# Performance work log

Measured on AMD Instinct MI355X. Metric: run time of the kernel, lower is better.

The kernel has to match this reference:

```python
import jax, jax.numpy as jnp
import numpy as np
from jax import lax

D_MODEL = 768
D_STATE = 64
BATCH = 2
SEQ = 2048


def setup_inputs() -> dict:
    key = jax.random.key(0)
    ks = jax.random.split(key, 12)
    d, n = D_MODEL, D_STATE
    x = jax.random.normal(ks[0], (BATCH, SEQ, d), dtype=jnp.float32)
    ln_gamma = jnp.ones((d,), jnp.float32)
    ln_beta = jnp.zeros((d,), jnp.float32)
    # nn.Linear default init ~ U(-1/sqrt(d), 1/sqrt(d))
    s = 1.0 / np.sqrt(d)
    W_in = jax.random.uniform(ks[1], (d, d), jnp.float32, -s, s)
    b_in = jax.random.uniform(ks[2], (d,), jnp.float32, -s, s)
    log_A = jax.random.normal(ks[3], (d, n), jnp.float32)
    B_p = jax.random.normal(ks[4], (d, n), jnp.float32) * 0.1
    C_p = jax.random.normal(ks[5], (d, n), jnp.float32) * 0.1
    D_p = jnp.ones((d,), jnp.float32)
    log_dt = jax.random.uniform(ks[6], (d,), jnp.float32) * 0.01 - 2.0
    W_out = jax.random.uniform(ks[7], (d, d), jnp.float32, -s, s)
    b_out = jax.random.uniform(ks[8], (d,), jnp.float32, -s, s)
    return {
        "x": x, "ln_gamma": ln_gamma, "ln_beta": ln_beta,
        "W_in": W_in, "b_in": b_in, "log_A": log_A,
        "B_p": B_p, "C_p": C_p, "D_p": D_p, "log_dt": log_dt,
        "W_out": W_out, "b_out": b_out,
    }


def reference(x, ln_gamma, ln_beta, W_in, b_in, log_A, B_p, C_p, D_p, log_dt, W_out, b_out):
    residual = x
    # LayerNorm (eps=1e-5, elementwise affine)
    mu = jnp.mean(x, axis=-1, keepdims=True)
    var = jnp.var(x, axis=-1, keepdims=True)
    xn = (x - mu) / jnp.sqrt(var + 1e-5) * ln_gamma + ln_beta
    # in_proj (torch Linear: x @ W^T + b)
    u = xn @ W_in.T + b_in  # [B,S,d]
    # Discretization
    A = -jnp.exp(log_A)                     # [d,N]
    dt = jnp.exp(log_dt)[:, None]           # [d,1]
    A_bar = jnp.exp(dt * A)                 # [d,N]
    B_bar = B_p * dt                        # [d,N]
    b, s, d = u.shape
    h0 = jnp.zeros((b, d, D_STATE), u.dtype)
    u_t = jnp.transpose(u, (1, 0, 2))       # [S,B,d]

    def step(h, xt):
        # h: [B,d,N], xt: [B,d]
        h = A_bar * h + B_bar * xt[:, :, None]
        y = jnp.einsum('bdn,dn->bd', h, C_p) + D_p * xt
        return h, y

    _, ys = lax.scan(step, h0, u_t)         # ys: [S,B,d]
    y = jnp.transpose(ys, (1, 0, 2))        # [B,S,d]
    y = y @ W_out.T + b_out
    # dropout is identity in eval mode
    return y + residual
```

## Files before the change

### kernel.cpp

```cpp
#include <hip/hip_runtime.h>
#include <math.h>

#define D_MODEL 768
#define D_STATE 64
#define BATCH   2
#define SEQ     2048
#define M_TOTAL (BATCH * SEQ)

typedef unsigned short ushort_t;
typedef float f32x4 __attribute__((ext_vector_type(4)));
typedef __bf16 bf16x8 __attribute__((ext_vector_type(8)));

__device__ __forceinline__ ushort_t f2bf(float f) {
    unsigned u = __float_as_uint(f);
    u = (u + 0x7FFFu + ((u >> 16) & 1u)) >> 16;
    return (ushort_t)u;
}

__device__ __forceinline__ void gload16(const void* g, void* shm) {
    __builtin_amdgcn_global_load_lds(
        (const __attribute__((address_space(1))) void*)g,
        (__attribute__((address_space(3))) void*)shm, 16, 0, 0);
}

__global__ __launch_bounds__(256) void pre_kernel(const float* __restrict__ x,
                                                  const float* __restrict__ gamma,
                                                  const float* __restrict__ beta,
                                                  ushort_t* __restrict__ xnb,
                                                  const float* __restrict__ W_in,
                                                  const float* __restrict__ W_out,
                                                  ushort_t* __restrict__ Winb,
                                                  ushort_t* __restrict__ Woutb) {
    int bx = blockIdx.x;
    if (bx >= 1024) {
        int b2 = bx - 1024;
        const float* src = (b2 < 576) ? W_in : W_out;
        ushort_t*    dst = (b2 < 576) ? Winb : Woutb;
        int blk = (b2 < 576) ? b2 : b2 - 576;
        int i = (blk * 256 + threadIdx.x) * 4;
        float4 v = *(const float4*)(src + i);
        ushort4 o = make_ushort4(f2bf(v.x), f2bf(v.y), f2bf(v.z), f2bf(v.w));
        *(ushort4*)(dst + i) = o;
        return;
    }
    int row  = bx * 4 + (threadIdx.x >> 6);
    int lane = threadIdx.x & 63;
    const float* xr = x + (size_t)row * D_MODEL;
    float4 v[3];
    v[0] = *(const float4*)(xr + lane * 4);
    v[1] = *(const float4*)(xr + 256 + lane * 4);
    v[2] = *(const float4*)(xr + 512 + lane * 4);
    float s = 0.f, ss = 0.f;
#pragma unroll
    for (int i = 0; i < 3; ++i) {
        s  += v[i].x + v[i].y + v[i].z + v[i].w;
        ss += v[i].x * v[i].x + v[i].y * v[i].y + v[i].z * v[i].z + v[i].w * v[i].w;
    }
#pragma unroll
    for (int off = 1; off < 64; off <<= 1) {
        s  += __shfl_xor(s, off, 64);
        ss += __shfl_xor(ss, off, 64);
    }
    float mean = s * (1.0f / 768.0f);
    float var  = ss * (1.0f / 768.0f) - mean * mean;
    float inv  = 1.0f / sqrtf(var + 1e-5f);
    ushort_t* xo = xnb + (size_t)row * D_MODEL;
#pragma unroll
    for (int i = 0; i < 3; ++i) {
        int c = i * 256 + lane * 4;
        float4 g  = *(const float4*)(gamma + c);
        float4 bb = *(const float4*)(beta + c);
        ushort4 o = make_ushort4(f2bf((v[i].x - mean) * inv * g.x + bb.x),
                                 f2bf((v[i].y - mean) * inv * g.y + bb.y),
                                 f2bf((v[i].z - mean) * inv * g.z + bb.z),
                                 f2bf((v[i].w - mean) * inv * g.w + bb.w));
        *(ushort4*)(xo + c) = o;
    }
}


__global__ __launch_bounds__(256) void gemm_in(const ushort_t* __restrict__ A,
                                               const ushort_t* __restrict__ B,
                                               const float* __restrict__ bias,
                                               ushort_t* __restrict__ uTb) {
    __shared__ __align__(16) char smem[40960];
    float* T = (float*)smem;

    int tid = threadIdx.x;
    int w = tid >> 6, l = tid & 63;
    int bm = blockIdx.x * 64, bn = blockIdx.y * 96;
    int wr = w >> 1, wc = w & 1;

    int lr = l >> 3;
    int scol0 = ((l & 7) ^ lr) * 8;

    float biasv[3];
#pragma unroll
    for (int nt = 0; nt < 3; ++nt)
        biasv[nt] = bias[bn + wc * 48 + nt * 16 + (l & 15)];

    char* Acur = smem;          char* Aalt = smem + 8192;
    char* Bcur = smem + 16384;  char* Balt = smem + 28672;

#pragma unroll
    for (int q = 0; q < 2; ++q) {
        int row = w * 16 + q * 8 + lr;
        gload16(A + (size_t)(bm + row) * D_MODEL + scol0, Acur + w * 2048 + q * 1024);
    }
#pragma unroll
    for (int q = 0; q < 3; ++q) {
        int row = w * 24 + q * 8 + lr;
        gload16(B + (size_t)(bn + row) * D_MODEL + scol0, Bcur + w * 3072 + q * 1024);
    }
    __syncthreads();

    f32x4 acc[2][3] = {};
    for (int t = 0; t < 12; ++t) {
        if (t < 11) {
            int k1 = (t + 1) * 64;
#pragma unroll
            for (int q = 0; q < 2; ++q) {
                int row = w * 16 + q * 8 + lr;
                gload16(A + (size_t)(bm + row) * D_MODEL + k1 + scol0, Aalt + w * 2048 + q * 1024);
            }
#pragma unroll
            for (int q = 0; q < 3; ++q) {
                int row = w * 24 + q * 8 + lr;
                gload16(B + (size_t)(bn + row) * D_MODEL + k1 + scol0, Balt + w * 3072 + q * 1024);
            }
        }
#pragma unroll
        for (int kk = 0; kk < 2; ++kk) {
            int sgb = kk * 4 + (l >> 4);
            bf16x8 af[2], bfr[3];
#pragma unroll
            for (int mt = 0; mt < 2; ++mt) {
                int r = wr * 32 + mt * 16 + (l & 15);
                af[mt] = *(const bf16x8*)(Acur + r * 128 + ((sgb ^ (r & 7)) * 16));
            }
#pragma unroll
            for (int nt = 0; nt < 3; ++nt) {
                int r = wc * 48 + nt * 16 + (l & 15);
                bfr[nt] = *(const bf16x8*)(Bcur + r * 128 + ((sgb ^ (r & 7)) * 16));
            }
#pragma unroll
            for (int mt = 0; mt < 2; ++mt)
#pragma unroll
                for (int nt = 0; nt < 3; ++nt)
                    acc[mt][nt] = __builtin_amdgcn_mfma_f32_16x16x32_bf16(af[mt], bfr[nt], acc[mt][nt], 0, 0, 0);
        }
        __syncthreads();
        char* t1 = Acur; Acur = Aalt; Aalt = t1;
        t1 = Bcur; Bcur = Balt; Balt = t1;
    }

#pragma unroll
    for (int mt = 0; mt < 2; ++mt)
#pragma unroll
        for (int nt = 0; nt < 3; ++nt)
#pragma unroll
            for (int i = 0; i < 4; ++i) {
                int nl = wc * 48 + nt * 16 + (l & 15);
                int ml = wr * 32 + mt * 16 + (l >> 4) * 4 + i;
                T[nl * 68 + ml] = acc[mt][nt][i] + biasv[nt];
            }
    __syncthreads();
    int b = bm >> 11, sbase = bm & 2047;
    for (int t2 = tid; t2 < 384; t2 += 256) {
        int n2 = t2 >> 2, m0 = (t2 & 3) * 16;
        ushort_t* dst = uTb + ((size_t)b * D_MODEL + bn + n2) * SEQ + sbase + m0;
#pragma unroll
        for (int q = 0; q < 4; ++q) {
            float4 v = *(const float4*)&T[n2 * 68 + m0 + q * 4];
            ushort4 o = make_ushort4(f2bf(v.x), f2bf(v.y), f2bf(v.z), f2bf(v.w));
            *(ushort4*)(dst + q * 4) = o;
        }
    }
}

__global__ __launch_bounds__(256) void gemm_out(const ushort_t* __restrict__ Y,
                                                const ushort_t* __restrict__ B,
                                                const float* __restrict__ bias,
                                                const float* __restrict__ resid,
                                                float* __restrict__ out) {
    __shared__ __align__(16) char smem[40960];
    int tid = threadIdx.x;
    int w = tid >> 6, l = tid & 63;
    int bm = blockIdx.x * 64, bn = blockIdx.y * 96;
    int wr = w >> 1, wc = w & 1;

    int bb = bm >> 11, sbase = bm & 2047;

    int lr = l >> 3;
    int scol0 = ((l & 7) ^ lr) * 8;

    int d0 = (tid & 31) * 2;
    int sq = (tid >> 5) * 8;
    int segd = d0 >> 3;
    int dby = (d0 & 7) * 2;

    float biasv[3];
#pragma unroll
    for (int nt = 0; nt < 3; ++nt)
        biasv[nt] = bias[bn + wc * 48 + nt * 16 + (l & 15)];

    char* Acur = smem;          char* Aalt = smem + 8192;
    char* Bcur = smem + 16384;  char* Balt = smem + 28672;

    {
        const ushort_t* yrow = Y + ((size_t)bb * D_MODEL + d0) * SEQ + sbase + sq;
        uint4 r0 = *(const uint4*)(yrow);
        uint4 r1 = *(const uint4*)(yrow + SEQ);
        const ushort_t* p0 = (const ushort_t*)&r0;
        const ushort_t* p1 = (const ushort_t*)&r1;
#pragma unroll
        for (int i = 0; i < 8; ++i) {
            int s = sq + i;
            unsigned pk = (unsigned)p0[i] | ((unsigned)p1[i] << 16);
            *(unsigned*)(Acur + s * 128 + ((segd ^ (s & 7)) * 16) + dby) = pk;
        }
#pragma unroll
        for (int q = 0; q < 3; ++q) {
            int row = w * 24 + q * 8 + lr;
            gload16(B + (size_t)(bn + row) * D_MODEL + scol0, Bcur + w * 3072 + q * 1024);
        }
    }
    __syncthreads();

    f32x4 acc[2][3] = {};
    for (int t = 0; t < 12; ++t) {
        uint4 r0, r1;
        if (t < 11) {
            int k1 = (t + 1) * 64;
            const ushort_t* yrow = Y + ((size_t)bb * D_MODEL + k1 + d0) * SEQ + sbase + sq;
            r0 = *(const uint4*)(yrow);
            r1 = *(const uint4*)(yrow + SEQ);
#pragma unroll
            for (int q = 0; q < 3; ++q) {
                int row = w * 24 + q * 8 + lr;
                gload16(B + (size_t)(bn + row) * D_MODEL + k1 + scol0, Balt + w * 3072 + q * 1024);
            }
        }
#pragma unroll
        for (int kk = 0; kk < 2; ++kk) {
            int sgb = kk * 4 + (l >> 4);
            bf16x8 af[2], bfr[3];
#pragma unroll
            for (int mt = 0; mt < 2; ++mt) {
                int r = wr * 32 + mt * 16 + (l & 15);
                af[mt] = *(const bf16x8*)(Acur + r * 128 + ((sgb ^ (r & 7)) * 16));
            }
#pragma unroll
            for (int nt = 0; nt < 3; ++nt) {
                int r = wc * 48 + nt * 16 + (l & 15);
                bfr[nt] = *(const bf16x8*)(Bcur + r * 128 + ((sgb ^ (r & 7)) * 16));
            }
#pragma unroll
            for (int mt = 0; mt < 2; ++mt)
#pragma unroll
                for (int nt = 0; nt < 3; ++nt)
                    acc[mt][nt] = __builtin_amdgcn_mfma_f32_16x16x32_bf16(af[mt], bfr[nt], acc[mt][nt], 0, 0, 0);
        }
        if (t < 11) {
            const ushort_t* p0 = (const ushort_t*)&r0;
            const ushort_t* p1 = (const ushort_t*)&r1;
#pragma unroll
            for (int i = 0; i < 8; ++i) {
                int s = sq + i;
                unsigned pk = (unsigned)p0[i] | ((unsigned)p1[i] << 16);
                *(unsigned*)(Aalt + s * 128 + ((segd ^ (s & 7)) * 16) + dby) = pk;
            }
        }
        __syncthreads();
        char* t1 = Acur; Acur = Aalt; Aalt = t1;
        t1 = Bcur; Bcur = Balt; Balt = t1;
    }

#pragma unroll
    for (int mt = 0; mt < 2; ++mt)
#pragma unroll
        for (int i = 0; i < 4; ++i) {
            int m = bm + wr * 32 + mt * 16 + (l >> 4) * 4 + i;
            const float* rp = resid + (size_t)m * D_MODEL + bn;
            float* op = out + (size_t)m * D_MODEL + bn;
#pragma unroll
            for (int nt = 0; nt < 3; ++nt) {
                int nl = wc * 48 + nt * 16 + (l & 15);
                op[nl] = acc[mt][nt][i] + biasv[nt] + rp[nl];
            }
        }
}

#define OFF_U  0
#define OFF_V  9216
#define OFF_T  18432
#define OFF_M  27648
#define OFF_H  36864
#define OFF_W  46080
#define OFF_SM 63488

__global__ __launch_bounds__(256) void scan_mm(const ushort_t* __restrict__ uTb,
                                               const float* __restrict__ log_A,
                                               const float* __restrict__ B_p,
                                               const float* __restrict__ C_p,
                                               const float* __restrict__ D_p,
                                               const float* __restrict__ log_dt,
                                               ushort_t* __restrict__ yTb) {
    __shared__ __align__(16) char smem[65024];
    ushort_t* Up = (ushort_t*)(smem + OFF_U);
    ushort_t* Vp = (ushort_t*)(smem + OFF_V);
    ushort_t* Tp = (ushort_t*)(smem + OFF_T);
    ushort_t* Mp = (ushort_t*)(smem + OFF_M);
    ushort_t* Hp = (ushort_t*)(smem + OFF_H);
    float*    Wp = (float*)(smem + OFF_W);
    float*    Kp = (float*)(smem + OFF_W);
    float*    aArr  = (float*)(smem + OFF_SM);
    float*    BbArr = aArr + 64;
    float*    CcArr = aArr + 128;
    float*    CBArr = aArr + 192;
    float*    Kc    = aArr + 256;

    int d   = blockIdx.x;
    int tid = threadIdx.x;
    int w   = tid >> 6, l = tid & 63;

    int r_pre = tid >> 2, seg_pre = (tid & 3) * 16;
    int bu_pre = r_pre >> 5, cu_pre = r_pre & 31;
    const ushort_t* usrc = uTb + ((size_t)bu_pre * D_MODEL + d) * SEQ + cu_pre * 64 + seg_pre;
    uint4 u01 = *(const uint4*)(usrc);
    uint4 u23 = *(const uint4*)(usrc + 8);

    if (tid < 64) {
        int n = tid;
        float dt = __expf(log_dt[d]);
        float a  = -dt * __expf(log_A[d * 64 + n]);
        float Bb = B_p[d * 64 + n] * dt;
        float Cc = C_p[d * 64 + n];
        aArr[n] = a; BbArr[n] = Bb; CcArr[n] = Cc; CBArr[n] = Cc * Bb;
    }
    __syncthreads();

    {
        int tau = tid & 63, part = tid >> 6;
        float s = 0.f;
#pragma unroll
        for (int i = 0; i < 16; ++i) {
            int n = part * 16 + i;
            s += CBArr[n] * __expf((float)tau * aArr[n]);
        }
        Kp[part * 64 + tau] = s;
    }
    __syncthreads();
    if (tid < 64)
        Kc[tid] = Kp[tid] + Kp[64 + tid] + Kp[128 + tid] + Kp[192 + tid]
                + (tid == 0 ? D_p[d] : 0.f);
    __syncthreads();

    {
        int r = tid >> 2, seg = (tid & 3) * 16;
        float a = aArr[r], Bb = BbArr[r];
#pragma unroll
        for (int i = 0; i < 16; ++i) {
            int s = seg + i;
            Vp[r * 72 + s] = f2bf(Bb * __expf((float)(63 - s) * a));
        }
#pragma unroll
        for (int i = 0; i < 16; ++i) {
            int n = seg + i;
            Mp[r * 72 + n] = f2bf(CcArr[n] * __expf((float)(r + 1) * aArr[n]));
        }
#pragma unroll
        for (int i = 0; i < 16; ++i) {
            int s = seg + i;
            Tp[r * 72 + s] = (s <= r) ? f2bf(Kc[r - s]) : (ushort_t)0;
        }
        *(uint4*)(Up + r * 72 + seg)     = u01;
        *(uint4*)(Up + r * 72 + seg + 8) = u23;
    }
    __syncthreads();

    {
        int p0 = w * 16;
        f32x4 acc1[4] = {};
#pragma unroll
        for (int kk = 0; kk < 2; ++kk) {
            int koff = kk * 32 + (l >> 4) * 8;
            bf16x8 af = *(const bf16x8*)(Vp + (p0 + (l & 15)) * 72 + koff);
#pragma unroll
            for (int qt = 0; qt < 4; ++qt) {
                bf16x8 bf = *(const bf16x8*)(Up + (qt * 16 + (l & 15)) * 72 + koff);
                acc1[qt] = __builtin_amdgcn_mfma_f32_16x16x32_bf16(af, bf, acc1[qt], 0, 0, 0);
            }
        }
#pragma unroll
        for (int qt = 0; qt < 4; ++qt)
#pragma unroll
            for (int i = 0; i < 4; ++i)
                Wp[(qt * 16 + (l & 15)) * 68 + p0 + (l >> 4) * 4 + i] = acc1[qt][i];
    }
    __syncthreads();

    if (tid < 128) {
        int b2 = tid >> 6, n = tid & 63;
        float Ab64 = __expf(64.f * aArr[n]);
        float H = 0.f;
#pragma unroll
        for (int c = 0; c < 32; ++c) {
            int col = b2 * 32 + c;
            Hp[col * 72 + n] = f2bf(H);
            H = fmaf(Ab64, H, Wp[col * 68 + n]);
        }
    }
    __syncthreads();

    {
        int j0 = w * 16;
        f32x4 accY[4] = {};
#pragma unroll
        for (int kk = 0; kk < 2; ++kk) {
            int koff = kk * 32 + (l >> 4) * 8;
            bf16x8 at = *(const bf16x8*)(Tp + (j0 + (l & 15)) * 72 + koff);
            bf16x8 am = *(const bf16x8*)(Mp + (j0 + (l & 15)) * 72 + koff);
#pragma unroll
            for (int qt = 0; qt < 4; ++qt) {
                bf16x8 bu = *(const bf16x8*)(Up + (qt * 16 + (l & 15)) * 72 + koff);
                bf16x8 bh = *(const bf16x8*)(Hp + (qt * 16 + (l & 15)) * 72 + koff);
                accY[qt] = __builtin_amdgcn_mfma_f32_16x16x32_bf16(at, bu, accY[qt], 0, 0, 0);
                accY[qt] = __builtin_amdgcn_mfma_f32_16x16x32_bf16(am, bh, accY[qt], 0, 0, 0);
            }
        }
#pragma unroll
        for (int qt = 0; qt < 4; ++qt)
#pragma unroll
            for (int i = 0; i < 4; ++i)
                Wp[(qt * 16 + (l & 15)) * 68 + j0 + (l >> 4) * 4 + i] = accY[qt][i];
    }
    __syncthreads();

    {
        int col = tid >> 2, jseg = (tid & 3) * 16;
        int b3 = col >> 5, c3 = col & 31;
        ushort_t* dst = yTb + ((size_t)b3 * D_MODEL + d) * SEQ + c3 * 64 + jseg;
#pragma unroll
        for (int q = 0; q < 4; ++q) {
            f32x4 v = *(const f32x4*)(Wp + col * 68 + jseg + q * 4);
            ushort4 o = make_ushort4(f2bf(v.x), f2bf(v.y), f2bf(v.z), f2bf(v.w));
            *(ushort4*)(dst + q * 4) = o;
        }
    }
}

extern "C" void kernel_launch(void* const* d_in, const int* in_sizes, int n_in,
                              void* d_out, int out_size, void* d_ws, size_t ws_size,
                              hipStream_t stream) {
    const float* x        = (const float*)d_in[0];
    const float* ln_gamma = (const float*)d_in[1];
    const float* ln_beta  = (const float*)d_in[2];
    const float* W_in     = (const float*)d_in[3];
    const float* b_in     = (const float*)d_in[4];
    const float* log_A    = (const float*)d_in[5];
    const float* B_p      = (const float*)d_in[6];
    const float* C_p      = (const float*)d_in[7];
    const float* D_p      = (const float*)d_in[8];
    const float* log_dt   = (const float*)d_in[9];
    const float* W_out    = (const float*)d_in[10];
    const float* b_out    = (const float*)d_in[11];
    float* out = (float*)d_out;

    char* ws = (char*)d_ws;
    ushort_t* uTb   = (ushort_t*)(ws + 0);
    ushort_t* yTb   = (ushort_t*)(ws + 6291456);
    ushort_t* xnb   = (ushort_t*)(ws + 12582912);
    ushort_t* Winb  = (ushort_t*)(ws + 18874368);
    ushort_t* Woutb = (ushort_t*)(ws + 20054016);

    pre_kernel<<<dim3(1024 + 1152), 256, 0, stream>>>(x, ln_gamma, ln_beta, xnb,
                                                      W_in, W_out, Winb, Woutb);
    gemm_in<<<dim3(M_TOTAL / 64, D_MODEL / 96), 256, 0, stream>>>(xnb, Winb, b_in, uTb);
    scan_mm<<<dim3(D_MODEL), 256, 0, stream>>>(uTb, log_A, B_p, C_p, D_p, log_dt, yTb);
    gemm_out<<<dim3(M_TOTAL / 64, D_MODEL / 96), 256, 0, stream>>>(yTb, Woutb, b_out, x, out);
}
```

Measured before the change: 125.7 us.

## Fuse LayerNorm into input-projection GEMM A-tile loading

Drops the separate LayerNorm pass that wrote a bf16 normalized copy of x, and computes per-row mean and inverse std inside gemm_in. The A tiles are then normalized, cast to bf16 and written into the swizzled LDS layout on the fly, with register prefetch of the next k-tile. This removes the xnb write and re-read and shrinks the pre-pass to a weight cast. In exchange each of the 8 column blocks re-reads and re-normalizes the fp32 rows, costing extra global traffic and ALU work inside the GEMM loop.

```diff
diff --git a/kernel.cpp b/kernel.cpp
--- a/kernel.cpp
+++ b/kernel.cpp
@@ -23,68 +23,32 @@
         (__attribute__((address_space(3))) void*)shm, 16, 0, 0);
 }
 
-__global__ __launch_bounds__(256) void pre_kernel(const float* __restrict__ x,
-                                                  const float* __restrict__ gamma,
-                                                  const float* __restrict__ beta,
-                                                  ushort_t* __restrict__ xnb,
-                                                  const float* __restrict__ W_in,
-                                                  const float* __restrict__ W_out,
-                                                  ushort_t* __restrict__ Winb,
-                                                  ushort_t* __restrict__ Woutb) {
-    int bx = blockIdx.x;
-    if (bx >= 1024) {
-        int b2 = bx - 1024;
-        const float* src = (b2 < 576) ? W_in : W_out;
-        ushort_t*    dst = (b2 < 576) ? Winb : Woutb;
-        int blk = (b2 < 576) ? b2 : b2 - 576;
-        int i = (blk * 256 + threadIdx.x) * 4;
-        float4 v = *(const float4*)(src + i);
-        ushort4 o = make_ushort4(f2bf(v.x), f2bf(v.y), f2bf(v.z), f2bf(v.w));
-        *(ushort4*)(dst + i) = o;
-        return;
-    }
-    int row  = bx * 4 + (threadIdx.x >> 6);
-    int lane = threadIdx.x & 63;
-    const float* xr = x + (size_t)row * D_MODEL;
-    float4 v[3];
-    v[0] = *(const float4*)(xr + lane * 4);
-    v[1] = *(const float4*)(xr + 256 + lane * 4);
-    v[2] = *(const float4*)(xr + 512 + lane * 4);
-    float s = 0.f, ss = 0.f;
-#pragma unroll
-    for (int i = 0; i < 3; ++i) {
-        s  += v[i].x + v[i].y + v[i].z + v[i].w;
-        ss += v[i].x * v[i].x + v[i].y * v[i].y + v[i].z * v[i].z + v[i].w * v[i].w;
-    }
-#pragma unroll
-    for (int off = 1; off < 64; off <<= 1) {
-        s  += __shfl_xor(s, off, 64);
-        ss += __shfl_xor(ss, off, 64);
-    }
-    float mean = s * (1.0f / 768.0f);
-    float var  = ss * (1.0f / 768.0f) - mean * mean;
-    float inv  = 1.0f / sqrtf(var + 1e-5f);
-    ushort_t* xo = xnb + (size_t)row * D_MODEL;
-#pragma unroll
-    for (int i = 0; i < 3; ++i) {
-        int c = i * 256 + lane * 4;
-        float4 g  = *(const float4*)(gamma + c);
-        float4 bb = *(const float4*)(beta + c);
-        ushort4 o = make_ushort4(f2bf((v[i].x - mean) * inv * g.x + bb.x),
-                                 f2bf((v[i].y - mean) * inv * g.y + bb.y),
-                                 f2bf((v[i].z - mean) * inv * g.z + bb.z),
-                                 f2bf((v[i].w - mean) * inv * g.w + bb.w));
-        *(ushort4*)(xo + c) = o;
-    }
-}
-
-
-__global__ __launch_bounds__(256) void gemm_in(const ushort_t* __restrict__ A,
+__global__ __launch_bounds__(256) void wcast_kernel(const float* __restrict__ W_in,
+                                                    const float* __restrict__ W_out,
+                                                    ushort_t* __restrict__ Winb,
+                                                    ushort_t* __restrict__ Woutb) {
+    int b2 = blockIdx.x;
+    const float* src = (b2 < 576) ? W_in : W_out;
+    ushort_t*    dst = (b2 < 576) ? Winb : Woutb;
+    int blk = (b2 < 576) ? b2 : b2 - 576;
+    int i = (blk * 256 + threadIdx.x) * 4;
+    float4 v = *(const float4*)(src + i);
+    ushort4 o = make_ushort4(f2bf(v.x), f2bf(v.y), f2bf(v.z), f2bf(v.w));
+    *(ushort4*)(dst + i) = o;
+}
+
+__global__ __launch_bounds__(256) void gemm_in(const float* __restrict__ X,
+                                               const float* __restrict__ gamma,
+                                               const float* __restrict__ beta,
                                                const ushort_t* __restrict__ B,
                                                const float* __restrict__ bias,
                                                ushort_t* __restrict__ uTb) {
-    __shared__ __align__(16) char smem[40960];
-    float* T = (float*)smem;
+    __shared__ __align__(16) char smem[47616];
+    float* T  = (float*)smem;
+    float* Gl = (float*)(smem + 40960);
+    float* Bl = (float*)(smem + 44032);
+    float* Mn = (float*)(smem + 47104);
+    float* Iv = (float*)(smem + 47360);
 
     int tid = threadIdx.x;
     int w = tid >> 6, l = tid & 63;
@@ -94,6 +58,8 @@
     int lr = l >> 3;
     int scol0 = ((l & 7) ^ lr) * 8;
 
+    int ar = tid >> 2, c4 = tid & 3;
+
     float biasv[3];
 #pragma unroll
     for (int nt = 0; nt < 3; ++nt)
@@ -102,27 +68,77 @@
     char* Acur = smem;          char* Aalt = smem + 8192;
     char* Bcur = smem + 16384;  char* Balt = smem + 28672;
 
-#pragma unroll
-    for (int q = 0; q < 2; ++q) {
-        int row = w * 16 + q * 8 + lr;
-        gload16(A + (size_t)(bm + row) * D_MODEL + scol0, Acur + w * 2048 + q * 1024);
+    for (int i = tid; i < 384; i += 256) {
+        if (i < 192) ((float4*)Gl)[i] = ((const float4*)gamma)[i];
+        else         ((float4*)Bl)[i - 192] = ((const float4*)beta)[i - 192];
     }
 #pragma unroll
     for (int q = 0; q < 3; ++q) {
         int row = w * 24 + q * 8 + lr;
         gload16(B + (size_t)(bn + row) * D_MODEL + scol0, Bcur + w * 3072 + q * 1024);
     }
+    for (int rr = 0; rr < 16; ++rr) {
+        int row = w * 16 + rr;
+        const float* xr = X + (size_t)(bm + row) * D_MODEL;
+        float4 v0 = ((const float4*)xr)[l];
+        float4 v1 = ((const float4*)xr)[64 + l];
+        float4 v2 = ((const float4*)xr)[128 + l];
+        float s  = v0.x + v0.y + v0.z + v0.w + v1.x + v1.y + v1.z + v1.w + v2.x + v2.y + v2.z + v2.w;
+        float ss = v0.x*v0.x + v0.y*v0.y + v0.z*v0.z + v0.w*v0.w
+                 + v1.x*v1.x + v1.y*v1.y + v1.z*v1.z + v1.w*v1.w
+                 + v2.x*v2.x + v2.y*v2.y + v2.z*v2.z + v2.w*v2.w;
+#pragma unroll
+        for (int off = 1; off < 64; off <<= 1) {
+            s  += __shfl_xor(s, off, 64);
+            ss += __shfl_xor(ss, off, 64);
+        }
+        if (l == 0) {
+            float mean = s * (1.0f / 768.0f);
+            float var  = ss * (1.0f / 768.0f) - mean * mean;
+            Mn[row] = mean;
+            Iv[row] = 1.0f / sqrtf(var + 1e-5f);
+        }
+    }
+    __syncthreads();
+
+    {
+        const float* xs = X + (size_t)(bm + ar) * D_MODEL + c4 * 16;
+        float4 v[4];
+#pragma unroll
+        for (int j = 0; j < 4; ++j) v[j] = ((const float4*)xs)[j];
+        float mean = Mn[ar], inv = Iv[ar];
+        float4 g[4], bb[4];
+#pragma unroll
+        for (int j = 0; j < 4; ++j) {
+            g[j]  = *(const float4*)(Gl + c4 * 16 + j * 4);
+            bb[j] = *(const float4*)(Bl + c4 * 16 + j * 4);
+        }
+        unsigned pk[8];
+#pragma unroll
+        for (int j = 0; j < 4; ++j) {
+            unsigned lo0 = f2bf((v[j].x - mean) * inv * g[j].x + bb[j].x);
+            unsigned hi0 = f2bf((v[j].y - mean) * inv * g[j].y + bb[j].y);
+            unsigned lo1 = f2bf((v[j].z - mean) * inv * g[j].z + bb[j].z);
+            unsigned hi1 = f2bf((v[j].w - mean) * inv * g[j].w + bb[j].w);
+            pk[j * 2]     = lo0 | (hi0 << 16);
+            pk[j * 2 + 1] = lo1 | (hi1 << 16);
+        }
+        int sg0 = c4 * 2, sg1 = c4 * 2 + 1;
+        *(uint4*)(Acur + ar * 128 + ((sg0 ^ (ar & 7)) * 16)) = make_uint4(pk[0], pk[1], pk[2], pk[3]);
+        *(uint4*)(Acur + ar * 128 + ((sg1 ^ (ar & 7)) * 16)) = make_uint4(pk[4], pk[5], pk[6], pk[7]);
+    }
     __syncthreads();
 
     f32x4 acc[2][3] = {};
     for (int t = 0; t < 12; ++t) {
+        float4 v[4];
+        float mean, inv;
         if (t < 11) {
             int k1 = (t + 1) * 64;
-#pragma unroll
-            for (int q = 0; q < 2; ++q) {
-                int row = w * 16 + q * 8 + lr;
-                gload16(A + (size_t)(bm + row) * D_MODEL + k1 + scol0, Aalt + w * 2048 + q * 1024);
-            }
+            const float* xs = X + (size_t)(bm + ar) * D_MODEL + k1 + c4 * 16;
+#pragma unroll
+            for (int j = 0; j < 4; ++j) v[j] = ((const float4*)xs)[j];
+            mean = Mn[ar]; inv = Iv[ar];
 #pragma unroll
             for (int q = 0; q < 3; ++q) {
                 int row = w * 24 + q * 8 + lr;
@@ -148,6 +164,28 @@
 #pragma unroll
                 for (int nt = 0; nt < 3; ++nt)
                     acc[mt][nt] = __builtin_amdgcn_mfma_f32_16x16x32_bf16(af[mt], bfr[nt], acc[mt][nt], 0, 0, 0);
+        }
+        if (t < 11) {
+            int k1 = (t + 1) * 64;
+            float4 g[4], bb[4];
+#pragma unroll
+            for (int j = 0; j < 4; ++j) {
+                g[j]  = *(const float4*)(Gl + k1 + c4 * 16 + j * 4);
+                bb[j] = *(const float4*)(Bl + k1 + c4 * 16 + j * 4);
+            }
+            unsigned pk[8];
+#pragma unroll
+            for (int j = 0; j < 4; ++j) {
+                unsigned lo0 = f2bf((v[j].x - mean) * inv * g[j].x + bb[j].x);
+                unsigned hi0 = f2bf((v[j].y - mean) * inv * g[j].y + bb[j].y);
+                unsigned lo1 = f2bf((v[j].z - mean) * inv * g[j].z + bb[j].z);
+                unsigned hi1 = f2bf((v[j].w - mean) * inv * g[j].w + bb[j].w);
+                pk[j * 2]     = lo0 | (hi0 << 16);
+                pk[j * 2 + 1] = lo1 | (hi1 << 16);
+            }
+            int sg0 = c4 * 2, sg1 = c4 * 2 + 1;
+            *(uint4*)(Aalt + ar * 128 + ((sg0 ^ (ar & 7)) * 16)) = make_uint4(pk[0], pk[1], pk[2], pk[3]);
+            *(uint4*)(Aalt + ar * 128 + ((sg1 ^ (ar & 7)) * 16)) = make_uint4(pk[4], pk[5], pk[6], pk[7]);
         }
         __syncthreads();
         char* t1 = Acur; Acur = Aalt; Aalt = t1;
@@ -470,13 +508,11 @@
     char* ws = (char*)d_ws;
     ushort_t* uTb   = (ushort_t*)(ws + 0);
     ushort_t* yTb   = (ushort_t*)(ws + 6291456);
-    ushort_t* xnb   = (ushort_t*)(ws + 12582912);
-    ushort_t* Winb  = (ushort_t*)(ws + 18874368);
-    ushort_t* Woutb = (ushort_t*)(ws + 20054016);
-
-    pre_kernel<<<dim3(1024 + 1152), 256, 0, stream>>>(x, ln_gamma, ln_beta, xnb,
-                                                      W_in, W_out, Winb, Woutb);
-    gemm_in<<<dim3(M_TOTAL / 64, D_MODEL / 96), 256, 0, stream>>>(xnb, Winb, b_in, uTb);
+    ushort_t* Winb  = (ushort_t*)(ws + 12582912);
+    ushort_t* Woutb = (ushort_t*)(ws + 13762560);
+
+    wcast_kernel<<<dim3(1152), 256, 0, stream>>>(W_in, W_out, Winb, Woutb);
+    gemm_in<<<dim3(M_TOTAL / 64, D_MODEL / 96), 256, 0, stream>>>(x, ln_gamma, ln_beta, Winb, b_in, uTb);
     scan_mm<<<dim3(D_MODEL), 256, 0, stream>>>(uTb, log_A, B_p, C_p, D_p, log_dt, yTb);
     gemm_out<<<dim3(M_TOTAL / 64, D_MODEL / 96), 256, 0, stream>>>(yTb, Woutb, b_out, x, out);
 }
```

Result: slower. 137.9 us (+9.7%).
